# Kernel tuning notes

Hardware: AMD Instinct MI355X
Metric: run time of the kernel (lower is better)

The kernel has to match this reference:

```python
import jax, jax.numpy as jnp
import numpy as np
from math import factorial, sqrt, pi

LMAX, NSH = 2, 9
F = 64
N_RBF = 20
N_INTER = 2
N_ATOMS = 1000
N_PAIRS = 10000
CUTOFF = 5.0

# ---------- Clebsch-Gordan coefficients for real spherical harmonics ----------

def _cg_complex(l1, m1, l2, m2, l3, m3):
    # <l1 m1 l2 m2 | l3 m3> via Racah formula
    if m3 != m1 + m2 or not (abs(l1 - l2) <= l3 <= l1 + l2):
        return 0.0
    f = factorial
    pre = sqrt((2 * l3 + 1) * f(l3 + l1 - l2) * f(l3 - l1 + l2) * f(l1 + l2 - l3) / f(l1 + l2 + l3 + 1))
    pre *= sqrt(f(l3 + m3) * f(l3 - m3) * f(l1 - m1) * f(l1 + m1) * f(l2 - m2) * f(l2 + m2))
    s = 0.0
    for k in range(l1 + l2 - l3 + 1):
        d = [k, l1 + l2 - l3 - k, l1 - m1 - k, l2 + m2 - k, l3 - l2 + m1 + k, l3 - l1 - m2 + k]
        if min(d) < 0:
            continue
        s += (-1) ** k / np.prod([float(f(t)) for t in d])
    return pre * s

def _sh_indices(lmax):
    l = np.concatenate([np.full(2 * ll + 1, ll) for ll in range(lmax + 1)])
    m = np.concatenate([np.arange(-ll, ll + 1) for ll in range(lmax + 1)])
    return l, m

def _real_cg(lmax):
    lidx, midx = _sh_indices(lmax)
    n = (lmax + 1) ** 2
    cgc = np.zeros((n, n, n))
    for a in range(n):
        for b in range(n):
            for c in range(n):
                cgc[a, b, c] = _cg_complex(lidx[a], midx[a], lidx[b], midx[b], lidx[c], midx[c])
    # complex -> real spherical harmonic change of basis (per degree l)
    U = np.zeros((n, n), dtype=np.complex128)
    for ll in range(lmax + 1):
        base = ll * ll + ll
        U[base, base] = 1.0
        for m in range(1, ll + 1):
            U[base + m, base - m] = 1 / sqrt(2)
            U[base + m, base + m] = (-1) ** m / sqrt(2)
            U[base - m, base - m] = 1j / sqrt(2)
            U[base - m, base + m] = -1j * (-1) ** m / sqrt(2)
    cgr = np.einsum('ijk,ai,bj,ck->abc', cgc.astype(np.complex128), U, U, U.conj())
    parity = (-1.0) ** lidx
    mask = (parity[:, None, None] * parity[None, :, None]) == parity[None, None, :]
    cgr = np.real(cgr) * mask
    cgr = np.transpose(cgr, (2, 0, 1))  # [s_out, s_in(x), s_filter(Y)]
    s1, s2, s3 = np.nonzero(np.abs(cgr) > 1e-9)
    return s1, s2, s3, cgr[s1, s2, s3].astype(np.float32), lidx

_S1, _S2, _S3, _CGV, _LIDX = _real_cg(LMAX)
IDX1 = jnp.asarray(_S1)            # output sh channel per CG path
IDX2 = jnp.asarray(_S2)            # input-feature sh channel per CG path
IDX3 = jnp.asarray(_S3)            # Ylm sh channel per CG path
CGVAL = jnp.asarray(_CGV)          # CG value per path
WIDX = jnp.asarray(_LIDX[_S3])     # radial-filter degree per CG path
LIDX = jnp.asarray(_LIDX)          # degree of each of the 9 sh channels

# ---------- real spherical harmonics (lmax=2, orthonormal, m=-l..l order) ----------

def _rsh(u):
    x, y, z = u[:, 0], u[:, 1], u[:, 2]
    c1 = sqrt(3.0 / (4.0 * pi))
    c2 = 0.5 * sqrt(15.0 / pi)
    return jnp.stack([
        jnp.full_like(x, 0.5 / sqrt(pi)),
        c1 * y, c1 * z, c1 * x,
        c2 * x * y,
        c2 * y * z,
        0.25 * sqrt(5.0 / pi) * (3.0 * z * z - 1.0),
        c2 * x * z,
        0.25 * sqrt(15.0 / pi) * (x * x - y * y),
    ], axis=1)


def setup_inputs() -> dict:
    key = jax.random.key(0)
    ks = jax.random.split(key, 10)
    atomic_numbers = jax.random.randint(ks[0], (N_ATOMS,), 0, 100)
    r_ij = 1.5 * jax.random.normal(ks[1], (N_PAIRS, 3), dtype=jnp.float32)
    idx_i = jnp.sort(jax.random.randint(ks[2], (N_PAIRS,), 0, N_ATOMS))
    idx_j = jax.random.randint(ks[3], (N_PAIRS,), 0, N_ATOMS)
    emb = jax.random.normal(ks[4], (100, F), dtype=jnp.float32)
    def s(k, sh, fan):
        return jax.random.normal(k, sh, dtype=jnp.float32) / float(np.sqrt(fan))
    Wf = s(ks[5], (N_INTER, N_RBF, (LMAX + 1) * F), N_RBF)
    bf = jnp.zeros((N_INTER, (LMAX + 1) * F), jnp.float32)
    W1 = s(ks[6], (N_INTER, F, F), F)
    W2 = s(ks[7], (N_INTER, F, F), F)
    W3 = s(ks[8], (N_INTER, F, F), F)
    Wg = s(ks[9], (N_INTER, F, (LMAX + 1) * F), F)
    bg = jnp.zeros((N_INTER, (LMAX + 1) * F), jnp.float32)
    return dict(atomic_numbers=atomic_numbers, r_ij=r_ij, idx_i=idx_i, idx_j=idx_j,
                emb=emb, Wf=Wf, bf=bf, W1=W1, W2=W2, W3=W3, Wg=Wg, bg=bg)


def reference(atomic_numbers, r_ij, idx_i, idx_j, emb, Wf, bf, W1, W2, W3, Wg, bg):
    n_atoms = atomic_numbers.shape[0]
    d = jnp.linalg.norm(r_ij, axis=1, keepdims=True)          # [P,1]
    Yij = _rsh(r_ij / d)                                       # [P,9]
    offsets = jnp.linspace(0.0, CUTOFF, N_RBF)                 # GaussianRBF
    width = CUTOFF / (N_RBF - 1)
    radial = jnp.exp((-0.5 / (width * width)) * (d - offsets) ** 2)   # [P,n_rbf]
    cut = 0.5 * (jnp.cos(d * (pi / CUTOFF)) + 1.0) * (d < CUTOFF)     # [P,1]
    # nuclear embedding + scalar2rsh (zero-pad l>0 channels)
    x = jnp.zeros((n_atoms, NSH, F), emb.dtype).at[:, 0, :].set(emb[atomic_numbers])
    for t in range(N_INTER):
        # SO3Convolution
        Wij = (radial @ Wf[t] + bf[t]).reshape(-1, LMAX + 1, F) * cut[:, :, None]  # [P,lmax+1,F]
        xj = x[idx_j]                                                              # [P,9,F]
        v = xj[:, IDX2] * Yij[:, IDX3, None] * Wij[:, WIDX] * CGVAL[None, :, None]  # [P,nnz,F]
        yij = jnp.zeros_like(xj).at[:, IDX1].add(v)                                 # CG scatter
        dx = jax.ops.segment_sum(yij, idx_i, num_segments=n_atoms)                  # edge->node scatter
        # mixing1 + SO3TensorProduct
        ddx = dx @ W1[t]
        tp = jnp.zeros_like(dx).at[:, IDX1].add(dx[:, IDX2] * ddx[:, IDX3] * CGVAL[None, :, None])
        dx = (dx + tp) @ W2[t]
        # SO3ParametricGatedNonlinearity (gate from l=0 channel)
        gate = (dx[:, 0] @ Wg[t] + bg[t]).reshape(-1, LMAX + 1, F)
        dx = dx * jax.nn.sigmoid(gate[:, LIDX])
        dx = dx @ W3[t]
        x = x + dx
    return x  # multipole_representation [n_atoms, 9, F]; x[:,0] is scalar_representation
```

## Files before the change

kernel.cpp:

```cpp
#include <hip/hip_runtime.h>
#include <cmath>

constexpr int kNsh    = 9;
constexpr int kF      = 64;
constexpr int kNrbf   = 20;
constexpr int kNAtoms = 1000;
constexpr int kNPairs = 10000;
constexpr float kCutoffF = 5.0f;
constexpr int kMaxNZ  = 200;
constexpr int kCp     = 12;
constexpr int kXs     = kF * kCp;

struct CGSparse {
  int n;
  int c[kMaxNZ];
  int a[kMaxNZ];
  int b[kMaxNZ];
  float v[kMaxNZ];
};

constexpr double cfact(int n) {
  double r = 1.0;
  for (int i = 2; i <= n; i++) r *= (double)i;
  return r;
}
constexpr double cabs_(double x) { return x < 0 ? -x : x; }
constexpr double csqrt_(double x) {
  if (x <= 0.0) return 0.0;
  double g = x < 1.0 ? 1.0 : x;
  for (int i = 0; i < 60; i++) g = 0.5 * (g + x / g);
  return g;
}

constexpr double cg_cplx(int l1, int m1, int l2, int m2, int l3, int m3) {
  if (m3 != m1 + m2) return 0.0;
  int lo = l1 > l2 ? l1 - l2 : l2 - l1;
  if (l3 < lo || l3 > l1 + l2) return 0.0;
  double pre = csqrt_((2 * l3 + 1) * cfact(l3 + l1 - l2) * cfact(l3 - l1 + l2) *
                      cfact(l1 + l2 - l3) / cfact(l1 + l2 + l3 + 1));
  pre *= csqrt_(cfact(l3 + m3) * cfact(l3 - m3) * cfact(l1 - m1) *
                cfact(l1 + m1) * cfact(l2 - m2) * cfact(l2 + m2));
  double s = 0.0;
  for (int k = 0; k <= l1 + l2 - l3; k++) {
    int d0 = k, d1 = l1 + l2 - l3 - k, d2 = l1 - m1 - k;
    int d3 = l2 + m2 - k, d4 = l3 - l2 + m1 + k, d5 = l3 - l1 - m2 + k;
    if (d0 < 0 || d1 < 0 || d2 < 0 || d3 < 0 || d4 < 0 || d5 < 0) continue;
    double den = cfact(d0) * cfact(d1) * cfact(d2) * cfact(d3) * cfact(d4) * cfact(d5);
    s += ((k % 2) ? -1.0 : 1.0) / den;
  }
  return pre * s;
}

constexpr CGSparse build_cg() {
  CGSparse out{};
  int lidx[9] = {0, 1, 1, 1, 2, 2, 2, 2, 2};
  int midx[9] = {0, -1, 0, 1, -2, -1, 0, 1, 2};
  double Ur[9][9] = {};
  double Ui[9][9] = {};
  for (int l = 0; l <= 2; l++) {
    int base = l * l + l;
    Ur[base][base] = 1.0;
    for (int m = 1; m <= l; m++) {
      double s2 = 1.0 / csqrt_(2.0);
      double sgn = (m % 2) ? -1.0 : 1.0;
      Ur[base + m][base - m] = s2;
      Ur[base + m][base + m] = sgn * s2;
      Ui[base - m][base - m] = s2;
      Ui[base - m][base + m] = -sgn * s2;
    }
  }
  double cgr[9][9][9] = {};
  for (int i = 0; i < 9; i++)
    for (int j = 0; j < 9; j++)
      for (int k = 0; k < 9; k++) {
        double cv = cg_cplx(lidx[i], midx[i], lidx[j], midx[j], lidx[k], midx[k]);
        if (cv == 0.0) continue;
        for (int a2 = 0; a2 < 9; a2++) {
          if (Ur[a2][i] == 0.0 && Ui[a2][i] == 0.0) continue;
          for (int b2 = 0; b2 < 9; b2++) {
            if (Ur[b2][j] == 0.0 && Ui[b2][j] == 0.0) continue;
            for (int c2 = 0; c2 < 9; c2++) {
              if (Ur[c2][k] == 0.0 && Ui[c2][k] == 0.0) continue;
              double ar = Ur[a2][i], ai = Ui[a2][i];
              double br = Ur[b2][j], bi = Ui[b2][j];
              double cr = Ur[c2][k], ci = -Ui[c2][k];
              double pr = ar * br - ai * bi;
              double pi = ar * bi + ai * br;
              double rr = pr * cr - pi * ci;
              cgr[c2][a2][b2] += rr * cv;
            }
          }
        }
      }
  int n = 0;
  for (int c2 = 0; c2 < 9; c2++)
    for (int a2 = 0; a2 < 9; a2++)
      for (int b2 = 0; b2 < 9; b2++) {
        bool mask = ((lidx[a2] + lidx[b2]) % 2) == (lidx[c2] % 2);
        double v = mask ? cgr[c2][a2][b2] : 0.0;
        if (cabs_(v) > 1e-9) {
          out.c[n] = c2;
          out.a[n] = a2;
          out.b[n] = b2;
          out.v[n] = (float)v;
          n++;
        }
      }
  out.n = n;
  return out;
}

constexpr CGSparse CG = build_cg();
static_assert(CG.n > 0 && CG.n <= kMaxNZ, "CG table size out of range");

constexpr int kPreBlkPairs = kNPairs / 4;
constexpr int kPreBlkSeg   = (kNAtoms + 1 + 255) / 256;
constexpr int kPreBlkTotal = kPreBlkPairs + kPreBlkSeg;

__global__ __launch_bounds__(256) void k_pre(
    const float* __restrict__ rij, const float* __restrict__ Wf,
    const float* __restrict__ bf, const int* __restrict__ idx_i,
    float* __restrict__ Ypd, float* __restrict__ Wpair,
    int* __restrict__ seg) {
  const int blk = blockIdx.x;
  if (blk < kPreBlkPairs) {
    int wv = threadIdx.x >> 6;
    int f = threadIdx.x & 63;
    int p = blk * 4 + wv;
    float rx = rij[3 * p + 0], ry = rij[3 * p + 1], rz = rij[3 * p + 2];
    float d = sqrtf(rx * rx + ry * ry + rz * rz);
    float inv = 1.0f / d;
    float x = rx * inv, y = ry * inv, z = rz * inv;
    const float c0 = 0.28209479177387814f;
    const float c1 = 0.4886025119029199f;
    const float c2 = 1.0925484305920792f;
    const float c3 = 0.31539156525252005f;
    const float c4 = 0.5462742152960396f;
    if (f < 9) {
      float yv =
          (f == 0) ? c0 :
          (f == 1) ? c1 * y :
          (f == 2) ? c1 * z :
          (f == 3) ? c1 * x :
          (f == 4) ? c2 * x * y :
          (f == 5) ? c2 * y * z :
          (f == 6) ? c3 * (3.0f * z * z - 1.0f) :
          (f == 7) ? c2 * x * z :
                     c4 * (x * x - y * y);
      Ypd[p * 16 + f] = yv;
    }
    float cut = (d < kCutoffF) ? 0.5f * (cosf(d * (float)(M_PI / 5.0)) + 1.0f) : 0.0f;
    float radial[kNrbf];
    const float width = kCutoffF / (kNrbf - 1);
    const float coef = -0.5f / (width * width);
    #pragma unroll
    for (int k = 0; k < kNrbf; k++) {
      float off = (kCutoffF * k) / (kNrbf - 1);
      float tt = d - off;
      radial[k] = expf(coef * tt * tt);
    }
    #pragma unroll
    for (int t = 0; t < 2; t++) {
      #pragma unroll
      for (int l = 0; l < 3; l++) {
        float w = bf[t * 192 + l * 64 + f];
        #pragma unroll
        for (int k = 0; k < kNrbf; k++) {
          w += radial[k] * Wf[t * (kNrbf * 192) + k * 192 + l * 64 + f];
        }
        Wpair[t * (kNPairs * 192) + p * 192 + l * 64 + f] = w * cut;
      }
    }
  } else {
    int a = (blk - kPreBlkPairs) * 256 + threadIdx.x;
    if (a <= kNAtoms) {
      int lo = 0, hi = kNPairs;
      while (lo < hi) {
        int mid = (lo + hi) >> 1;
        if (idx_i[mid] < a) lo = mid + 1; else hi = mid;
      }
      seg[a] = lo;
    }
  }
}

__device__ __forceinline__ void mm_phase(const float* __restrict__ sA,
                                         const float* __restrict__ W,
                                         float* __restrict__ sRw,
                                         int k0, int cgi, int fb) {
  if (cgi >= 3) return;
  const int c0 = cgi * 4;
  float acc[4][4];
  #pragma unroll
  for (int i = 0; i < 4; i++)
    #pragma unroll
    for (int j = 0; j < 4; j++) acc[i][j] = 0.f;
  #pragma unroll
  for (int half = 0; half < 2; half++) {
    float4 wr[8];
    #pragma unroll
    for (int kk = 0; kk < 8; kk++) {
      wr[kk] = *(const float4*)(W + (k0 + half * 8 + kk) * kF + fb);
    }
    #pragma unroll
    for (int kk = 0; kk < 8; kk++) {
      int k = k0 + half * 8 + kk;
      float4 av = *(const float4*)(sA + k * kCp + c0);
      float4 wv = wr[kk];
      float a[4] = {av.x, av.y, av.z, av.w};
      float w[4] = {wv.x, wv.y, wv.z, wv.w};
      #pragma unroll
      for (int i = 0; i < 4; i++)
        #pragma unroll
        for (int j = 0; j < 4; j++) acc[i][j] += a[i] * w[j];
    }
  }
  #pragma unroll
  for (int j = 0; j < 4; j++) {
    float4 v = {acc[0][j], acc[1][j], acc[2][j], acc[3][j]};
    *(float4*)(sRw + (fb + j) * kCp + c0) = v;
  }
}

template <int T>
__global__ __launch_bounds__(256) void k_inter(
    const float* __restrict__ Ypd, const float* __restrict__ Wpt,
    const int* __restrict__ seg, const int* __restrict__ idx_j,
    const int* __restrict__ Z, const float* __restrict__ emb,
    const float* __restrict__ x_in, const float* __restrict__ W1,
    const float* __restrict__ W2, const float* __restrict__ W3,
    const float* __restrict__ Wg, const float* __restrict__ bg,
    float* __restrict__ x_out) {
  const int atom = blockIdx.x;
  const int tid = threadIdx.x;
  const int wv = tid >> 6;
  const int lane = tid & 63;
  const int cgi = lane >> 4;
  const int fb = (lane & 15) * 4;
  const int k0 = wv * 16;

  __shared__ __align__(16) float sA[kF * kCp];
  __shared__ __align__(16) float sR[4][kF * kCp];
  __shared__ __align__(16) float sGp[4][192];

  {
    float y[12];
    #pragma unroll
    for (int c = 0; c < 12; c++) y[c] = 0.f;
    const int s0 = seg[atom], s1 = seg[atom + 1];
    for (int p0 = s0 + wv; p0 < s1; p0 += 4) {
      const int p = __builtin_amdgcn_readfirstlane(p0);
      const int j = __builtin_amdgcn_readfirstlane(idx_j[p]);
      const float* Wp = Wpt + p * 192;
      float Wl0 = Wp[lane], Wl1 = Wp[64 + lane], Wl2 = Wp[128 + lane];
      const float* Yp = Ypd + p * 16;
      float YW[9];
      YW[0] = Yp[0] * Wl0;
      YW[1] = Yp[1] * Wl1;
      YW[2] = Yp[2] * Wl1;
      YW[3] = Yp[3] * Wl1;
      #pragma unroll
      for (int b = 4; b < 9; b++) YW[b] = Yp[b] * Wl2;
      if (T == 0) {
        float e = emb[Z[j] * kF + lane];
        #pragma unroll
        for (int q = 0; q < CG.n; q++) {
          if (CG.a[q] == 0) y[CG.c[q]] += CG.v[q] * YW[CG.b[q]] * e;
        }
      } else {
        const float* xj = x_in + j * kXs + lane * kCp;
        float xv[12];
        *(float4*)&xv[0] = *(const float4*)(xj + 0);
        *(float4*)&xv[4] = *(const float4*)(xj + 4);
        *(float4*)&xv[8] = *(const float4*)(xj + 8);
        #pragma unroll
        for (int q = 0; q < CG.n; q++) {
          y[CG.c[q]] += CG.v[q] * YW[CG.b[q]] * xv[CG.a[q]];
        }
      }
    }
    float4* r4 = (float4*)(sR[wv] + lane * kCp);
    r4[0] = *(float4*)&y[0];
    r4[1] = *(float4*)&y[4];
    r4[2] = *(float4*)&y[8];
  }
  __syncthreads();
  if (tid < 192) {
    const float4* r0 = (const float4*)sR[0];
    const float4* r1 = (const float4*)sR[1];
    const float4* r2 = (const float4*)sR[2];
    const float4* r3 = (const float4*)sR[3];
    float4 a = r0[tid], b = r1[tid], c = r2[tid], d = r3[tid];
    float4 s = {a.x + b.x + c.x + d.x, a.y + b.y + c.y + d.y,
                a.z + b.z + c.z + d.z, a.w + b.w + c.w + d.w};
    ((float4*)sA)[tid] = s;
  }
  __syncthreads();

  mm_phase(sA, W1, sR[wv], k0, cgi, fb);
  __syncthreads();

  if (wv == 0) {
    float dxv[12], ddx[12];
    {
      const float4* sa = (const float4*)(sA + lane * kCp);
      *(float4*)&dxv[0] = sa[0];
      *(float4*)&dxv[4] = sa[1];
      *(float4*)&dxv[8] = sa[2];
    }
    #pragma unroll
    for (int c = 0; c < 12; c++) {
      ddx[c] = sR[0][lane * kCp + c] + sR[1][lane * kCp + c] +
               sR[2][lane * kCp + c] + sR[3][lane * kCp + c];
    }
    float t2[12];
    #pragma unroll
    for (int c = 0; c < 9; c++) t2[c] = dxv[c];
    t2[9] = 0.f; t2[10] = 0.f; t2[11] = 0.f;
    #pragma unroll
    for (int q = 0; q < CG.n; q++) {
      t2[CG.c[q]] += CG.v[q] * dxv[CG.a[q]] * ddx[CG.b[q]];
    }
    float4* sa = (float4*)(sA + lane * kCp);
    sa[0] = *(float4*)&t2[0];
    sa[1] = *(float4*)&t2[4];
    sa[2] = *(float4*)&t2[8];
  }
  __syncthreads();

  mm_phase(sA, W2, sR[wv], k0, cgi, fb);
  __syncthreads();

  {
    float g0 = 0.f, g1 = 0.f, g2 = 0.f;
    #pragma unroll 4
    for (int kk = 0; kk < 16; kk++) {
      int k = k0 + kk;
      float a = sR[0][k * kCp] + sR[1][k * kCp] + sR[2][k * kCp] + sR[3][k * kCp];
      g0 += a * Wg[k * 192 + lane];
      g1 += a * Wg[k * 192 + 64 + lane];
      g2 += a * Wg[k * 192 + 128 + lane];
    }
    sGp[wv][lane] = g0;
    sGp[wv][64 + lane] = g1;
    sGp[wv][128 + lane] = g2;
  }
  __syncthreads();

  if (wv == 0) {
    float dx2v[12];
    #pragma unroll
    for (int c = 0; c < 12; c++) {
      dx2v[c] = sR[0][lane * kCp + c] + sR[1][lane * kCp + c] +
                sR[2][lane * kCp + c] + sR[3][lane * kCp + c];
    }
    float g0 = bg[lane] + sGp[0][lane] + sGp[1][lane] + sGp[2][lane] + sGp[3][lane];
    float g1 = bg[64 + lane] + sGp[0][64 + lane] + sGp[1][64 + lane] +
               sGp[2][64 + lane] + sGp[3][64 + lane];
    float g2 = bg[128 + lane] + sGp[0][128 + lane] + sGp[1][128 + lane] +
               sGp[2][128 + lane] + sGp[3][128 + lane];
    g0 = 1.f / (1.f + expf(-g0));
    g1 = 1.f / (1.f + expf(-g1));
    g2 = 1.f / (1.f + expf(-g2));
    float dx3[12];
    dx3[0] = dx2v[0] * g0;
    dx3[1] = dx2v[1] * g1;
    dx3[2] = dx2v[2] * g1;
    dx3[3] = dx2v[3] * g1;
    #pragma unroll
    for (int c = 4; c < 9; c++) dx3[c] = dx2v[c] * g2;
    dx3[9] = 0.f; dx3[10] = 0.f; dx3[11] = 0.f;
    float4* sa = (float4*)(sA + lane * kCp);
    sa[0] = *(float4*)&dx3[0];
    sa[1] = *(float4*)&dx3[4];
    sa[2] = *(float4*)&dx3[8];
  }
  __syncthreads();

  mm_phase(sA, W3, sR[wv], k0, cgi, fb);
  __syncthreads();

  if (T == 0) {
    if (tid < 192) {
      const int f = tid / 3, r = tid % 3;
      const float4* r0 = (const float4*)sR[0];
      const float4* r1 = (const float4*)sR[1];
      const float4* r2 = (const float4*)sR[2];
      const float4* r3 = (const float4*)sR[3];
      float4 a = r0[tid], b = r1[tid], c = r2[tid], d = r3[tid];
      float4 s = {a.x + b.x + c.x + d.x, a.y + b.y + c.y + d.y,
                  a.z + b.z + c.z + d.z, a.w + b.w + c.w + d.w};
      if (r == 0) s.x += emb[Z[atom] * kF + f];
      *(float4*)(x_out + atom * kXs + tid * 4) = s;
    }
  } else {
    if (tid < 192) {
      const float4* r0 = (const float4*)sR[0];
      const float4* r1 = (const float4*)sR[1];
      const float4* r2 = (const float4*)sR[2];
      const float4* r3 = (const float4*)sR[3];
      float4 a = r0[tid], b = r1[tid], c = r2[tid], d = r3[tid];
      float4 xi = *(const float4*)(x_in + atom * kXs + tid * 4);
      float4 s = {a.x + b.x + c.x + d.x + xi.x, a.y + b.y + c.y + d.y + xi.y,
                  a.z + b.z + c.z + d.z + xi.z, a.w + b.w + c.w + d.w + xi.w};
      ((float4*)sA)[tid] = s;
    }
    __syncthreads();
    #pragma unroll
    for (int r = 0; r < 3; r++) {
      int i = r * 256 + tid;
      if (i < kNsh * kF) {
        int c = i >> 6, f = i & 63;
        x_out[atom * (kNsh * kF) + i] = sA[f * kCp + c];
      }
    }
  }
}

extern "C" void kernel_launch(void* const* d_in, const int* in_sizes, int n_in,
                              void* d_out, int out_size, void* d_ws, size_t ws_size,
                              hipStream_t stream) {
  const int* Z        = (const int*)d_in[0];
  const float* rij    = (const float*)d_in[1];
  const int* idx_i    = (const int*)d_in[2];
  const int* idx_j    = (const int*)d_in[3];
  const float* emb    = (const float*)d_in[4];
  const float* Wf     = (const float*)d_in[5];
  const float* bf     = (const float*)d_in[6];
  const float* W1     = (const float*)d_in[7];
  const float* W2     = (const float*)d_in[8];
  const float* W3     = (const float*)d_in[9];
  const float* Wg     = (const float*)d_in[10];
  const float* bg     = (const float*)d_in[11];
  float* out = (float*)d_out;

  float* x1    = (float*)d_ws;
  float* Ypd   = x1 + kNAtoms * kXs;
  float* Wpair = Ypd + kNPairs * 16;
  int*   seg   = (int*)(Wpair + 2 * kNPairs * 192);

  k_pre<<<kPreBlkTotal, 256, 0, stream>>>(rij, Wf, bf, idx_i, Ypd, Wpair, seg);

  k_inter<0><<<kNAtoms, 256, 0, stream>>>(
      Ypd, Wpair, seg, idx_j, Z, emb, x1,
      W1, W2, W3, Wg, bg, x1);

  k_inter<1><<<kNAtoms, 256, 0, stream>>>(
      Ypd, Wpair + kNPairs * 192, seg, idx_j, Z, emb, x1,
      W1 + kF * kF, W2 + kF * kF, W3 + kF * kF,
      Wg + kF * 192, bg + 192, out);
}
```

Measured before the change: 125.6 us.

## Use eight waves per atom block and reduce matmul partials into shared buffer

Doubles the block size from 4 to 8 wavefronts per atom, so each wave handles every eighth pair in the edge gather and an 8-row K slice in each 64x64 mix. Partial results are now summed once by a dedicated reduction into a new shared buffer sB instead of being re-summed inside the single-wave CG and gate stages. This aims to spread the per-atom serial work across more waves. In exchange it adds extra barriers and roughly doubles shared memory per block, which may limit how many blocks fit on a CU.

```diff
diff --git a/kernel.cpp b/kernel.cpp
--- a/kernel.cpp
+++ b/kernel.cpp
@@ -10,6 +10,7 @@
 constexpr int kMaxNZ  = 200;
 constexpr int kCp     = 12;
 constexpr int kXs     = kF * kCp;
+constexpr int kNW     = 8;
 
 struct CGSparse {
   int n;
@@ -197,14 +198,14 @@
     for (int j = 0; j < 4; j++) acc[i][j] = 0.f;
   #pragma unroll
   for (int half = 0; half < 2; half++) {
-    float4 wr[8];
-    #pragma unroll
-    for (int kk = 0; kk < 8; kk++) {
-      wr[kk] = *(const float4*)(W + (k0 + half * 8 + kk) * kF + fb);
-    }
-    #pragma unroll
-    for (int kk = 0; kk < 8; kk++) {
-      int k = k0 + half * 8 + kk;
+    float4 wr[4];
+    #pragma unroll
+    for (int kk = 0; kk < 4; kk++) {
+      wr[kk] = *(const float4*)(W + (k0 + half * 4 + kk) * kF + fb);
+    }
+    #pragma unroll
+    for (int kk = 0; kk < 4; kk++) {
+      int k = k0 + half * 4 + kk;
       float4 av = *(const float4*)(sA + k * kCp + c0);
       float4 wv = wr[kk];
       float a[4] = {av.x, av.y, av.z, av.w};
@@ -222,8 +223,22 @@
   }
 }
 
+__device__ __forceinline__ void reduce_partials(const float (*sR)[kF * kCp],
+                                                float* __restrict__ dst,
+                                                int tid) {
+  if (tid < 192) {
+    float4 s = ((const float4*)sR[0])[tid];
+    #pragma unroll
+    for (int w = 1; w < kNW; w++) {
+      float4 v = ((const float4*)sR[w])[tid];
+      s.x += v.x; s.y += v.y; s.z += v.z; s.w += v.w;
+    }
+    ((float4*)dst)[tid] = s;
+  }
+}
+
 template <int T>
-__global__ __launch_bounds__(256) void k_inter(
+__global__ __launch_bounds__(512, 6) void k_inter(
     const float* __restrict__ Ypd, const float* __restrict__ Wpt,
     const int* __restrict__ seg, const int* __restrict__ idx_j,
     const int* __restrict__ Z, const float* __restrict__ emb,
@@ -237,18 +252,19 @@
   const int lane = tid & 63;
   const int cgi = lane >> 4;
   const int fb = (lane & 15) * 4;
-  const int k0 = wv * 16;
+  const int k0 = wv * 8;
 
   __shared__ __align__(16) float sA[kF * kCp];
-  __shared__ __align__(16) float sR[4][kF * kCp];
-  __shared__ __align__(16) float sGp[4][192];
+  __shared__ __align__(16) float sB[kF * kCp];
+  __shared__ __align__(16) float sR[kNW][kF * kCp];
+  __shared__ __align__(16) float sGp[kNW][192];
 
   {
     float y[12];
     #pragma unroll
     for (int c = 0; c < 12; c++) y[c] = 0.f;
     const int s0 = seg[atom], s1 = seg[atom + 1];
-    for (int p0 = s0 + wv; p0 < s1; p0 += 4) {
+    for (int p0 = s0 + wv; p0 < s1; p0 += kNW) {
       const int p = __builtin_amdgcn_readfirstlane(p0);
       const int j = __builtin_amdgcn_readfirstlane(idx_j[p]);
       const float* Wp = Wpt + p * 192;
@@ -285,19 +301,12 @@
     r4[2] = *(float4*)&y[8];
   }
   __syncthreads();
-  if (tid < 192) {
-    const float4* r0 = (const float4*)sR[0];
-    const float4* r1 = (const float4*)sR[1];
-    const float4* r2 = (const float4*)sR[2];
-    const float4* r3 = (const float4*)sR[3];
-    float4 a = r0[tid], b = r1[tid], c = r2[tid], d = r3[tid];
-    float4 s = {a.x + b.x + c.x + d.x, a.y + b.y + c.y + d.y,
-                a.z + b.z + c.z + d.z, a.w + b.w + c.w + d.w};
-    ((float4*)sA)[tid] = s;
-  }
+  reduce_partials(sR, sA, tid);
   __syncthreads();
 
   mm_phase(sA, W1, sR[wv], k0, cgi, fb);
+  __syncthreads();
+  reduce_partials(sR, sB, tid);
   __syncthreads();
 
   if (wv == 0) {
@@ -307,11 +316,10 @@
       *(float4*)&dxv[0] = sa[0];
       *(float4*)&dxv[4] = sa[1];
       *(float4*)&dxv[8] = sa[2];
-    }
-    #pragma unroll
-    for (int c = 0; c < 12; c++) {
-      ddx[c] = sR[0][lane * kCp + c] + sR[1][lane * kCp + c] +
-               sR[2][lane * kCp + c] + sR[3][lane * kCp + c];
+      const float4* sb = (const float4*)(sB + lane * kCp);
+      *(float4*)&ddx[0] = sb[0];
+      *(float4*)&ddx[4] = sb[1];
+      *(float4*)&ddx[8] = sb[2];
     }
     float t2[12];
     #pragma unroll
@@ -330,13 +338,15 @@
 
   mm_phase(sA, W2, sR[wv], k0, cgi, fb);
   __syncthreads();
+  reduce_partials(sR, sB, tid);
+  __syncthreads();
 
   {
     float g0 = 0.f, g1 = 0.f, g2 = 0.f;
-    #pragma unroll 4
-    for (int kk = 0; kk < 16; kk++) {
+    #pragma unroll
+    for (int kk = 0; kk < 8; kk++) {
       int k = k0 + kk;
-      float a = sR[0][k * kCp] + sR[1][k * kCp] + sR[2][k * kCp] + sR[3][k * kCp];
+      float a = sB[k * kCp];
       g0 += a * Wg[k * 192 + lane];
       g1 += a * Wg[k * 192 + 64 + lane];
       g2 += a * Wg[k * 192 + 128 + lane];
@@ -349,16 +359,19 @@
 
   if (wv == 0) {
     float dx2v[12];
-    #pragma unroll
-    for (int c = 0; c < 12; c++) {
-      dx2v[c] = sR[0][lane * kCp + c] + sR[1][lane * kCp + c] +
-                sR[2][lane * kCp + c] + sR[3][lane * kCp + c];
-    }
-    float g0 = bg[lane] + sGp[0][lane] + sGp[1][lane] + sGp[2][lane] + sGp[3][lane];
-    float g1 = bg[64 + lane] + sGp[0][64 + lane] + sGp[1][64 + lane] +
-               sGp[2][64 + lane] + sGp[3][64 + lane];
-    float g2 = bg[128 + lane] + sGp[0][128 + lane] + sGp[1][128 + lane] +
-               sGp[2][128 + lane] + sGp[3][128 + lane];
+    {
+      const float4* sb = (const float4*)(sB + lane * kCp);
+      *(float4*)&dx2v[0] = sb[0];
+      *(float4*)&dx2v[4] = sb[1];
+      *(float4*)&dx2v[8] = sb[2];
+    }
+    float g0 = bg[lane], g1 = bg[64 + lane], g2 = bg[128 + lane];
+    #pragma unroll
+    for (int w = 0; w < kNW; w++) {
+      g0 += sGp[w][lane];
+      g1 += sGp[w][64 + lane];
+      g2 += sGp[w][128 + lane];
+    }
     g0 = 1.f / (1.f + expf(-g0));
     g1 = 1.f / (1.f + expf(-g1));
     g2 = 1.f / (1.f + expf(-g2));
@@ -383,32 +396,31 @@
   if (T == 0) {
     if (tid < 192) {
       const int f = tid / 3, r = tid % 3;
-      const float4* r0 = (const float4*)sR[0];
-      const float4* r1 = (const float4*)sR[1];
-      const float4* r2 = (const float4*)sR[2];
-      const float4* r3 = (const float4*)sR[3];
-      float4 a = r0[tid], b = r1[tid], c = r2[tid], d = r3[tid];
-      float4 s = {a.x + b.x + c.x + d.x, a.y + b.y + c.y + d.y,
-                  a.z + b.z + c.z + d.z, a.w + b.w + c.w + d.w};
+      float4 s = ((const float4*)sR[0])[tid];
+      #pragma unroll
+      for (int w = 1; w < kNW; w++) {
+        float4 v = ((const float4*)sR[w])[tid];
+        s.x += v.x; s.y += v.y; s.z += v.z; s.w += v.w;
+      }
       if (r == 0) s.x += emb[Z[atom] * kF + f];
       *(float4*)(x_out + atom * kXs + tid * 4) = s;
     }
   } else {
     if (tid < 192) {
-      const float4* r0 = (const float4*)sR[0];
-      const float4* r1 = (const float4*)sR[1];
-      const float4* r2 = (const float4*)sR[2];
-      const float4* r3 = (const float4*)sR[3];
-      float4 a = r0[tid], b = r1[tid], c = r2[tid], d = r3[tid];
+      float4 s = ((const float4*)sR[0])[tid];
+      #pragma unroll
+      for (int w = 1; w < kNW; w++) {
+        float4 v = ((const float4*)sR[w])[tid];
+        s.x += v.x; s.y += v.y; s.z += v.z; s.w += v.w;
+      }
       float4 xi = *(const float4*)(x_in + atom * kXs + tid * 4);
-      float4 s = {a.x + b.x + c.x + d.x + xi.x, a.y + b.y + c.y + d.y + xi.y,
-                  a.z + b.z + c.z + d.z + xi.z, a.w + b.w + c.w + d.w + xi.w};
+      s.x += xi.x; s.y += xi.y; s.z += xi.z; s.w += xi.w;
       ((float4*)sA)[tid] = s;
     }
     __syncthreads();
     #pragma unroll
-    for (int r = 0; r < 3; r++) {
-      int i = r * 256 + tid;
+    for (int r = 0; r < 2; r++) {
+      int i = r * 512 + tid;
       if (i < kNsh * kF) {
         int c = i >> 6, f = i & 63;
         x_out[atom * (kNsh * kF) + i] = sA[f * kCp + c];
@@ -441,11 +453,11 @@
 
   k_pre<<<kPreBlkTotal, 256, 0, stream>>>(rij, Wf, bf, idx_i, Ypd, Wpair, seg);
 
-  k_inter<0><<<kNAtoms, 256, 0, stream>>>(
+  k_inter<0><<<kNAtoms, 512, 0, stream>>>(
       Ypd, Wpair, seg, idx_j, Z, emb, x1,
       W1, W2, W3, Wg, bg, x1);
 
-  k_inter<1><<<kNAtoms, 256, 0, stream>>>(
+  k_inter<1><<<kNAtoms, 512, 0, stream>>>(
       Ypd, Wpair + kNPairs * 192, seg, idx_j, Z, emb, x1,
       W1 + kF * kF, W2 + kF * kF, W3 + kF * kF,
       Wg + kF * 192, bg + 192, out);
```

After: 134.3 us. 1.07x slower.

## Fuse pair precompute into first interaction kernel, dropping a launch

Applied to the files above, without the earlier changes.

The separate pre-pass kernel is removed. The first interaction kernel now computes the spherical harmonics, cutoff and radial filter weights for its own atom's pairs, and extra blocks build the segment table. Each atom block finds its pair range with its own binary search over idx_i. This saves one kernel launch and the global round-trip for the first-layer filters. In exchange, the per-pair radial work is spread unevenly across atom blocks, and Wpair/Ypd are still written to and read back from global memory within the same block.

```diff
diff --git a/kernel.cpp b/kernel.cpp
--- a/kernel.cpp
+++ b/kernel.cpp
@@ -113,77 +113,6 @@
 constexpr CGSparse CG = build_cg();
 static_assert(CG.n > 0 && CG.n <= kMaxNZ, "CG table size out of range");
 
-constexpr int kPreBlkPairs = kNPairs / 4;
-constexpr int kPreBlkSeg   = (kNAtoms + 1 + 255) / 256;
-constexpr int kPreBlkTotal = kPreBlkPairs + kPreBlkSeg;
-
-__global__ __launch_bounds__(256) void k_pre(
-    const float* __restrict__ rij, const float* __restrict__ Wf,
-    const float* __restrict__ bf, const int* __restrict__ idx_i,
-    float* __restrict__ Ypd, float* __restrict__ Wpair,
-    int* __restrict__ seg) {
-  const int blk = blockIdx.x;
-  if (blk < kPreBlkPairs) {
-    int wv = threadIdx.x >> 6;
-    int f = threadIdx.x & 63;
-    int p = blk * 4 + wv;
-    float rx = rij[3 * p + 0], ry = rij[3 * p + 1], rz = rij[3 * p + 2];
-    float d = sqrtf(rx * rx + ry * ry + rz * rz);
-    float inv = 1.0f / d;
-    float x = rx * inv, y = ry * inv, z = rz * inv;
-    const float c0 = 0.28209479177387814f;
-    const float c1 = 0.4886025119029199f;
-    const float c2 = 1.0925484305920792f;
-    const float c3 = 0.31539156525252005f;
-    const float c4 = 0.5462742152960396f;
-    if (f < 9) {
-      float yv =
-          (f == 0) ? c0 :
-          (f == 1) ? c1 * y :
-          (f == 2) ? c1 * z :
-          (f == 3) ? c1 * x :
-          (f == 4) ? c2 * x * y :
-          (f == 5) ? c2 * y * z :
-          (f == 6) ? c3 * (3.0f * z * z - 1.0f) :
-          (f == 7) ? c2 * x * z :
-                     c4 * (x * x - y * y);
-      Ypd[p * 16 + f] = yv;
-    }
-    float cut = (d < kCutoffF) ? 0.5f * (cosf(d * (float)(M_PI / 5.0)) + 1.0f) : 0.0f;
-    float radial[kNrbf];
-    const float width = kCutoffF / (kNrbf - 1);
-    const float coef = -0.5f / (width * width);
-    #pragma unroll
-    for (int k = 0; k < kNrbf; k++) {
-      float off = (kCutoffF * k) / (kNrbf - 1);
-      float tt = d - off;
-      radial[k] = expf(coef * tt * tt);
-    }
-    #pragma unroll
-    for (int t = 0; t < 2; t++) {
-      #pragma unroll
-      for (int l = 0; l < 3; l++) {
-        float w = bf[t * 192 + l * 64 + f];
-        #pragma unroll
-        for (int k = 0; k < kNrbf; k++) {
-          w += radial[k] * Wf[t * (kNrbf * 192) + k * 192 + l * 64 + f];
-        }
-        Wpair[t * (kNPairs * 192) + p * 192 + l * 64 + f] = w * cut;
-      }
-    }
-  } else {
-    int a = (blk - kPreBlkPairs) * 256 + threadIdx.x;
-    if (a <= kNAtoms) {
-      int lo = 0, hi = kNPairs;
-      while (lo < hi) {
-        int mid = (lo + hi) >> 1;
-        if (idx_i[mid] < a) lo = mid + 1; else hi = mid;
-      }
-      seg[a] = lo;
-    }
-  }
-}
-
 __device__ __forceinline__ void mm_phase(const float* __restrict__ sA,
                                          const float* __restrict__ W,
                                          float* __restrict__ sRw,
@@ -222,11 +151,245 @@
   }
 }
 
-template <int T>
-__global__ __launch_bounds__(256) void k_inter(
+__global__ __launch_bounds__(256) void k_interA(
+    const float* __restrict__ rij, const float* __restrict__ Wf,
+    const float* __restrict__ bf, const int* __restrict__ idx_i,
+    const int* __restrict__ idx_j, const int* __restrict__ Z,
+    const float* __restrict__ emb, const float* __restrict__ W1,
+    const float* __restrict__ W2, const float* __restrict__ W3,
+    const float* __restrict__ Wg, const float* __restrict__ bg,
+    float* __restrict__ Ypd, float* __restrict__ Wpair,
+    int* __restrict__ seg, float* __restrict__ x_out) {
+  const int blk = blockIdx.x;
+  const int tid = threadIdx.x;
+
+  if (blk >= kNAtoms) {
+    int a = (blk - kNAtoms) * 256 + tid;
+    if (a <= kNAtoms) {
+      int lo = 0, hi = kNPairs;
+      while (lo < hi) {
+        int mid = (lo + hi) >> 1;
+        if (idx_i[mid] < a) lo = mid + 1; else hi = mid;
+      }
+      seg[a] = lo;
+    }
+    return;
+  }
+
+  const int atom = blk;
+  const int wv = tid >> 6;
+  const int lane = tid & 63;
+  const int cgi = lane >> 4;
+  const int fb = (lane & 15) * 4;
+  const int k0 = wv * 16;
+
+  __shared__ __align__(16) float sA[kF * kCp];
+  __shared__ __align__(16) float sR[4][kF * kCp];
+  __shared__ __align__(16) float sGp[4][192];
+  __shared__ int ss[2];
+
+  if (tid < 2) {
+    int target = atom + tid;
+    int lo = 0, hi = kNPairs;
+    while (lo < hi) {
+      int mid = (lo + hi) >> 1;
+      if (idx_i[mid] < target) lo = mid + 1; else hi = mid;
+    }
+    ss[tid] = lo;
+  }
+  __syncthreads();
+  const int s0 = ss[0], s1 = ss[1];
+
+  for (int p0 = s0 + wv; p0 < s1; p0 += 4) {
+    const int p = __builtin_amdgcn_readfirstlane(p0);
+    float rx = rij[3 * p + 0], ry = rij[3 * p + 1], rz = rij[3 * p + 2];
+    float d = sqrtf(rx * rx + ry * ry + rz * rz);
+    float inv = 1.0f / d;
+    float x = rx * inv, y = ry * inv, z = rz * inv;
+    const float c0 = 0.28209479177387814f;
+    const float c1 = 0.4886025119029199f;
+    const float c2 = 1.0925484305920792f;
+    const float c3 = 0.31539156525252005f;
+    const float c4 = 0.5462742152960396f;
+    if (lane < 9) {
+      float yv =
+          (lane == 0) ? c0 :
+          (lane == 1) ? c1 * y :
+          (lane == 2) ? c1 * z :
+          (lane == 3) ? c1 * x :
+          (lane == 4) ? c2 * x * y :
+          (lane == 5) ? c2 * y * z :
+          (lane == 6) ? c3 * (3.0f * z * z - 1.0f) :
+          (lane == 7) ? c2 * x * z :
+                        c4 * (x * x - y * y);
+      Ypd[p * 16 + lane] = yv;
+    }
+    float cut = (d < kCutoffF) ? 0.5f * (cosf(d * (float)(M_PI / 5.0)) + 1.0f) : 0.0f;
+    float radial[kNrbf];
+    const float width = kCutoffF / (kNrbf - 1);
+    const float coef = -0.5f / (width * width);
+    #pragma unroll
+    for (int k = 0; k < kNrbf; k++) {
+      float off = (kCutoffF * k) / (kNrbf - 1);
+      float tt = d - off;
+      radial[k] = expf(coef * tt * tt);
+    }
+    #pragma unroll
+    for (int t = 0; t < 2; t++) {
+      #pragma unroll
+      for (int l = 0; l < 3; l++) {
+        float w = bf[t * 192 + l * 64 + lane];
+        #pragma unroll
+        for (int k = 0; k < kNrbf; k++) {
+          w += radial[k] * Wf[t * (kNrbf * 192) + k * 192 + l * 64 + lane];
+        }
+        Wpair[t * (kNPairs * 192) + p * 192 + l * 64 + lane] = w * cut;
+      }
+    }
+  }
+  __syncthreads();
+
+  {
+    float y[12];
+    #pragma unroll
+    for (int c = 0; c < 12; c++) y[c] = 0.f;
+    for (int p0 = s0 + wv; p0 < s1; p0 += 4) {
+      const int p = __builtin_amdgcn_readfirstlane(p0);
+      const int j = __builtin_amdgcn_readfirstlane(idx_j[p]);
+      const float* Wp = Wpair + p * 192;
+      float Wl0 = Wp[lane], Wl1 = Wp[64 + lane], Wl2 = Wp[128 + lane];
+      const float* Yp = Ypd + p * 16;
+      float YW[9];
+      YW[0] = Yp[0] * Wl0;
+      YW[1] = Yp[1] * Wl1;
+      YW[2] = Yp[2] * Wl1;
+      YW[3] = Yp[3] * Wl1;
+      #pragma unroll
+      for (int b = 4; b < 9; b++) YW[b] = Yp[b] * Wl2;
+      float e = emb[Z[j] * kF + lane];
+      #pragma unroll
+      for (int q = 0; q < CG.n; q++) {
+        if (CG.a[q] == 0) y[CG.c[q]] += CG.v[q] * YW[CG.b[q]] * e;
+      }
+    }
+    float4* r4 = (float4*)(sR[wv] + lane * kCp);
+    r4[0] = *(float4*)&y[0];
+    r4[1] = *(float4*)&y[4];
+    r4[2] = *(float4*)&y[8];
+  }
+  __syncthreads();
+  if (tid < 192) {
+    const float4* r0 = (const float4*)sR[0];
+    const float4* r1 = (const float4*)sR[1];
+    const float4* r2 = (const float4*)sR[2];
+    const float4* r3 = (const float4*)sR[3];
+    float4 a = r0[tid], b = r1[tid], c = r2[tid], d = r3[tid];
+    float4 s = {a.x + b.x + c.x + d.x, a.y + b.y + c.y + d.y,
+                a.z + b.z + c.z + d.z, a.w + b.w + c.w + d.w};
+    ((float4*)sA)[tid] = s;
+  }
+  __syncthreads();
+
+  mm_phase(sA, W1, sR[wv], k0, cgi, fb);
+  __syncthreads();
+
+  if (wv == 0) {
+    float dxv[12], ddx[12];
+    {
+      const float4* sa = (const float4*)(sA + lane * kCp);
+      *(float4*)&dxv[0] = sa[0];
+      *(float4*)&dxv[4] = sa[1];
+      *(float4*)&dxv[8] = sa[2];
+    }
+    #pragma unroll
+    for (int c = 0; c < 12; c++) {
+      ddx[c] = sR[0][lane * kCp + c] + sR[1][lane * kCp + c] +
+               sR[2][lane * kCp + c] + sR[3][lane * kCp + c];
+    }
+    float t2[12];
+    #pragma unroll
+    for (int c = 0; c < 9; c++) t2[c] = dxv[c];
+    t2[9] = 0.f; t2[10] = 0.f; t2[11] = 0.f;
+    #pragma unroll
+    for (int q = 0; q < CG.n; q++) {
+      t2[CG.c[q]] += CG.v[q] * dxv[CG.a[q]] * ddx[CG.b[q]];
+    }
+    float4* sa = (float4*)(sA + lane * kCp);
+    sa[0] = *(float4*)&t2[0];
+    sa[1] = *(float4*)&t2[4];
+    sa[2] = *(float4*)&t2[8];
+  }
+  __syncthreads();
+
+  mm_phase(sA, W2, sR[wv], k0, cgi, fb);
+  __syncthreads();
+
+  {
+    float g0 = 0.f, g1 = 0.f, g2 = 0.f;
+    #pragma unroll 4
+    for (int kk = 0; kk < 16; kk++) {
+      int k = k0 + kk;
+      float a = sR[0][k * kCp] + sR[1][k * kCp] + sR[2][k * kCp] + sR[3][k * kCp];
+      g0 += a * Wg[k * 192 + lane];
+      g1 += a * Wg[k * 192 + 64 + lane];
+      g2 += a * Wg[k * 192 + 128 + lane];
+    }
+    sGp[wv][lane] = g0;
+    sGp[wv][64 + lane] = g1;
+    sGp[wv][128 + lane] = g2;
+  }
+  __syncthreads();
+
+  if (wv == 0) {
+    float dx2v[12];
+    #pragma unroll
+    for (int c = 0; c < 12; c++) {
+      dx2v[c] = sR[0][lane * kCp + c] + sR[1][lane * kCp + c] +
+                sR[2][lane * kCp + c] + sR[3][lane * kCp + c];
+    }
+    float g0 = bg[lane] + sGp[0][lane] + sGp[1][lane] + sGp[2][lane] + sGp[3][lane];
+    float g1 = bg[64 + lane] + sGp[0][64 + lane] + sGp[1][64 + lane] +
+               sGp[2][64 + lane] + sGp[3][64 + lane];
+    float g2 = bg[128 + lane] + sGp[0][128 + lane] + sGp[1][128 + lane] +
+               sGp[2][128 + lane] + sGp[3][128 + lane];
+    g0 = 1.f / (1.f + expf(-g0));
+    g1 = 1.f / (1.f + expf(-g1));
+    g2 = 1.f / (1.f + expf(-g2));
+    float dx3[12];
+    dx3[0] = dx2v[0] * g0;
+    dx3[1] = dx2v[1] * g1;
+    dx3[2] = dx2v[2] * g1;
+    dx3[3] = dx2v[3] * g1;
+    #pragma unroll
+    for (int c = 4; c < 9; c++) dx3[c] = dx2v[c] * g2;
+    dx3[9] = 0.f; dx3[10] = 0.f; dx3[11] = 0.f;
+    float4* sa = (float4*)(sA + lane * kCp);
+    sa[0] = *(float4*)&dx3[0];
+    sa[1] = *(float4*)&dx3[4];
+    sa[2] = *(float4*)&dx3[8];
+  }
+  __syncthreads();
+
+  mm_phase(sA, W3, sR[wv], k0, cgi, fb);
+  __syncthreads();
+
+  if (tid < 192) {
+    const int f = tid / 3, r = tid % 3;
+    const float4* r0 = (const float4*)sR[0];
+    const float4* r1 = (const float4*)sR[1];
+    const float4* r2 = (const float4*)sR[2];
+    const float4* r3 = (const float4*)sR[3];
+    float4 a = r0[tid], b = r1[tid], c = r2[tid], d = r3[tid];
+    float4 s = {a.x + b.x + c.x + d.x, a.y + b.y + c.y + d.y,
+                a.z + b.z + c.z + d.z, a.w + b.w + c.w + d.w};
+    if (r == 0) s.x += emb[Z[atom] * kF + f];
+    *(float4*)(x_out + atom * kXs + tid * 4) = s;
+  }
+}
+
+__global__ __launch_bounds__(256) void k_interB(
     const float* __restrict__ Ypd, const float* __restrict__ Wpt,
     const int* __restrict__ seg, const int* __restrict__ idx_j,
-    const int* __restrict__ Z, const float* __restrict__ emb,
     const float* __restrict__ x_in, const float* __restrict__ W1,
     const float* __restrict__ W2, const float* __restrict__ W3,
     const float* __restrict__ Wg, const float* __restrict__ bg,
@@ -261,22 +424,14 @@
       YW[3] = Yp[3] * Wl1;
       #pragma unroll
       for (int b = 4; b < 9; b++) YW[b] = Yp[b] * Wl2;
-      if (T == 0) {
-        float e = emb[Z[j] * kF + lane];
-        #pragma unroll
-        for (int q = 0; q < CG.n; q++) {
-          if (CG.a[q] == 0) y[CG.c[q]] += CG.v[q] * YW[CG.b[q]] * e;
-        }
-      } else {
-        const float* xj = x_in + j * kXs + lane * kCp;
-        float xv[12];
-        *(float4*)&xv[0] = *(const float4*)(xj + 0);
-        *(float4*)&xv[4] = *(const float4*)(xj + 4);
-        *(float4*)&xv[8] = *(const float4*)(xj + 8);
-        #pragma unroll
-        for (int q = 0; q < CG.n; q++) {
-          y[CG.c[q]] += CG.v[q] * YW[CG.b[q]] * xv[CG.a[q]];
-        }
+      const float* xj = x_in + j * kXs + lane * kCp;
+      float xv[12];
+      *(float4*)&xv[0] = *(const float4*)(xj + 0);
+      *(float4*)&xv[4] = *(const float4*)(xj + 4);
+      *(float4*)&xv[8] = *(const float4*)(xj + 8);
+      #pragma unroll
+      for (int q = 0; q < CG.n; q++) {
+        y[CG.c[q]] += CG.v[q] * YW[CG.b[q]] * xv[CG.a[q]];
       }
     }
     float4* r4 = (float4*)(sR[wv] + lane * kCp);
@@ -380,39 +535,24 @@
   mm_phase(sA, W3, sR[wv], k0, cgi, fb);
   __syncthreads();
 
-  if (T == 0) {
-    if (tid < 192) {
-      const int f = tid / 3, r = tid % 3;
-      const float4* r0 = (const float4*)sR[0];
-      const float4* r1 = (const float4*)sR[1];
-      const float4* r2 = (const float4*)sR[2];
-      const float4* r3 = (const float4*)sR[3];
-      float4 a = r0[tid], b = r1[tid], c = r2[tid], d = r3[tid];
-      float4 s = {a.x + b.x + c.x + d.x, a.y + b.y + c.y + d.y,
-                  a.z + b.z + c.z + d.z, a.w + b.w + c.w + d.w};
-      if (r == 0) s.x += emb[Z[atom] * kF + f];
-      *(float4*)(x_out + atom * kXs + tid * 4) = s;
-    }
-  } else {
-    if (tid < 192) {
-      const float4* r0 = (const float4*)sR[0];
-      const float4* r1 = (const float4*)sR[1];
-      const float4* r2 = (const float4*)sR[2];
-      const float4* r3 = (const float4*)sR[3];
-      float4 a = r0[tid], b = r1[tid], c = r2[tid], d = r3[tid];
-      float4 xi = *(const float4*)(x_in + atom * kXs + tid * 4);
-      float4 s = {a.x + b.x + c.x + d.x + xi.x, a.y + b.y + c.y + d.y + xi.y,
-                  a.z + b.z + c.z + d.z + xi.z, a.w + b.w + c.w + d.w + xi.w};
-      ((float4*)sA)[tid] = s;
-    }
-    __syncthreads();
-    #pragma unroll
-    for (int r = 0; r < 3; r++) {
-      int i = r * 256 + tid;
-      if (i < kNsh * kF) {
-        int c = i >> 6, f = i & 63;
-        x_out[atom * (kNsh * kF) + i] = sA[f * kCp + c];
-      }
+  if (tid < 192) {
+    const float4* r0 = (const float4*)sR[0];
+    const float4* r1 = (const float4*)sR[1];
+    const float4* r2 = (const float4*)sR[2];
+    const float4* r3 = (const float4*)sR[3];
+    float4 a = r0[tid], b = r1[tid], c = r2[tid], d = r3[tid];
+    float4 xi = *(const float4*)(x_in + atom * kXs + tid * 4);
+    float4 s = {a.x + b.x + c.x + d.x + xi.x, a.y + b.y + c.y + d.y + xi.y,
+                a.z + b.z + c.z + d.z + xi.z, a.w + b.w + c.w + d.w + xi.w};
+    ((float4*)sA)[tid] = s;
+  }
+  __syncthreads();
+  #pragma unroll
+  for (int r = 0; r < 3; r++) {
+    int i = r * 256 + tid;
+    if (i < kNsh * kF) {
+      int c = i >> 6, f = i & 63;
+      x_out[atom * (kNsh * kF) + i] = sA[f * kCp + c];
     }
   }
 }
@@ -439,14 +579,12 @@
   float* Wpair = Ypd + kNPairs * 16;
   int*   seg   = (int*)(Wpair + 2 * kNPairs * 192);
 
-  k_pre<<<kPreBlkTotal, 256, 0, stream>>>(rij, Wf, bf, idx_i, Ypd, Wpair, seg);
-
-  k_inter<0><<<kNAtoms, 256, 0, stream>>>(
-      Ypd, Wpair, seg, idx_j, Z, emb, x1,
-      W1, W2, W3, Wg, bg, x1);
-
-  k_inter<1><<<kNAtoms, 256, 0, stream>>>(
-      Ypd, Wpair + kNPairs * 192, seg, idx_j, Z, emb, x1,
+  k_interA<<<kNAtoms + 4, 256, 0, stream>>>(
+      rij, Wf, bf, idx_i, idx_j, Z, emb,
+      W1, W2, W3, Wg, bg, Ypd, Wpair, seg, x1);
+
+  k_interB<<<kNAtoms, 256, 0, stream>>>(
+      Ypd, Wpair + kNPairs * 192, seg, idx_j, x1,
       W1 + kF * kF, W2 + kF * kF, W3 + kF * kF,
       Wg + kF * 192, bg + 192, out);
 }
```

New measurement: 136.5 us. +8.7%, slower.

## Compute per-pair radial filter weights inside interaction kernels instead of precomputing

Applied to the files above, without the earlier changes.

The precompute kernel no longer materializes the per-pair filter weights for both interactions (two arrays of pairs×192 floats). It now stores only the spherical harmonics, the cutoff value and the cutoff-scaled radial basis per pair (32 floats). Each interaction block stages its filter matrix Wf in shared memory and recomputes the 192 filter weights per pair with a 20-term dot product. This trades a large global write and read for extra FLOPs and LDS traffic, and the larger shared-memory footprint may lower occupancy.

```diff
diff --git a/kernel.cpp b/kernel.cpp
--- a/kernel.cpp
+++ b/kernel.cpp
@@ -118,10 +118,8 @@
 constexpr int kPreBlkTotal = kPreBlkPairs + kPreBlkSeg;
 
 __global__ __launch_bounds__(256) void k_pre(
-    const float* __restrict__ rij, const float* __restrict__ Wf,
-    const float* __restrict__ bf, const int* __restrict__ idx_i,
-    float* __restrict__ Ypd, float* __restrict__ Wpair,
-    int* __restrict__ seg) {
+    const float* __restrict__ rij, const int* __restrict__ idx_i,
+    float* __restrict__ pd_all, int* __restrict__ seg) {
   const int blk = blockIdx.x;
   if (blk < kPreBlkPairs) {
     int wv = threadIdx.x >> 6;
@@ -136,8 +134,10 @@
     const float c2 = 1.0925484305920792f;
     const float c3 = 0.31539156525252005f;
     const float c4 = 0.5462742152960396f;
+    float cut = (d < kCutoffF) ? 0.5f * (cosf(d * (float)(M_PI / 5.0)) + 1.0f) : 0.0f;
+    float val = 0.f;
     if (f < 9) {
-      float yv =
+      val =
           (f == 0) ? c0 :
           (f == 1) ? c1 * y :
           (f == 2) ? c1 * z :
@@ -147,30 +147,16 @@
           (f == 6) ? c3 * (3.0f * z * z - 1.0f) :
           (f == 7) ? c2 * x * z :
                      c4 * (x * x - y * y);
-      Ypd[p * 16 + f] = yv;
-    }
-    float cut = (d < kCutoffF) ? 0.5f * (cosf(d * (float)(M_PI / 5.0)) + 1.0f) : 0.0f;
-    float radial[kNrbf];
-    const float width = kCutoffF / (kNrbf - 1);
-    const float coef = -0.5f / (width * width);
-    #pragma unroll
-    for (int k = 0; k < kNrbf; k++) {
-      float off = (kCutoffF * k) / (kNrbf - 1);
+    } else if (f == 9) {
+      val = cut;
+    } else if (f < 30) {
+      const float width = kCutoffF / (kNrbf - 1);
+      const float coef = -0.5f / (width * width);
+      float off = (kCutoffF * (f - 10)) / (kNrbf - 1);
       float tt = d - off;
-      radial[k] = expf(coef * tt * tt);
-    }
-    #pragma unroll
-    for (int t = 0; t < 2; t++) {
-      #pragma unroll
-      for (int l = 0; l < 3; l++) {
-        float w = bf[t * 192 + l * 64 + f];
-        #pragma unroll
-        for (int k = 0; k < kNrbf; k++) {
-          w += radial[k] * Wf[t * (kNrbf * 192) + k * 192 + l * 64 + f];
-        }
-        Wpair[t * (kNPairs * 192) + p * 192 + l * 64 + f] = w * cut;
-      }
-    }
+      val = expf(coef * tt * tt) * cut;
+    }
+    if (f < 30) pd_all[p * 32 + f] = val;
   } else {
     int a = (blk - kPreBlkPairs) * 256 + threadIdx.x;
     if (a <= kNAtoms) {
@@ -184,7 +170,7 @@
   }
 }
 
-__device__ __forceinline__ void mm_phase(const float* __restrict__ sA,
+__device__ __forceinline__ void mm_phase(const float* __restrict__ sIn,
                                          const float* __restrict__ W,
                                          float* __restrict__ sRw,
                                          int k0, int cgi, int fb) {
@@ -205,7 +191,7 @@
     #pragma unroll
     for (int kk = 0; kk < 8; kk++) {
       int k = k0 + half * 8 + kk;
-      float4 av = *(const float4*)(sA + k * kCp + c0);
+      float4 av = *(const float4*)(sIn + k * kCp + c0);
       float4 wv = wr[kk];
       float a[4] = {av.x, av.y, av.z, av.w};
       float w[4] = {wv.x, wv.y, wv.z, wv.w};
@@ -224,13 +210,13 @@
 
 template <int T>
 __global__ __launch_bounds__(256) void k_inter(
-    const float* __restrict__ Ypd, const float* __restrict__ Wpt,
-    const int* __restrict__ seg, const int* __restrict__ idx_j,
-    const int* __restrict__ Z, const float* __restrict__ emb,
-    const float* __restrict__ x_in, const float* __restrict__ W1,
-    const float* __restrict__ W2, const float* __restrict__ W3,
-    const float* __restrict__ Wg, const float* __restrict__ bg,
-    float* __restrict__ x_out) {
+    const float* __restrict__ pd_all, const float* __restrict__ Wft,
+    const float* __restrict__ bft, const int* __restrict__ seg,
+    const int* __restrict__ idx_j, const int* __restrict__ Z,
+    const float* __restrict__ emb, const float* __restrict__ x_in,
+    const float* __restrict__ W1, const float* __restrict__ W2,
+    const float* __restrict__ W3, const float* __restrict__ Wg,
+    const float* __restrict__ bg, float* __restrict__ x_out) {
   const int atom = blockIdx.x;
   const int tid = threadIdx.x;
   const int wv = tid >> 6;
@@ -239,9 +225,22 @@
   const int fb = (lane & 15) * 4;
   const int k0 = wv * 16;
 
+  __shared__ __align__(16) float sWf[kNrbf * 192];
   __shared__ __align__(16) float sA[kF * kCp];
   __shared__ __align__(16) float sR[4][kF * kCp];
   __shared__ __align__(16) float sGp[4][192];
+
+  {
+    const float4* g4 = (const float4*)Wft;
+    float4* s4 = (float4*)sWf;
+    #pragma unroll
+    for (int r = 0; r < 4; r++) {
+      int i = r * 256 + tid;
+      if (i < kNrbf * 192 / 4) s4[i] = g4[i];
+    }
+  }
+  const float bf0 = bft[lane], bf1 = bft[64 + lane], bf2 = bft[128 + lane];
+  __syncthreads();
 
   {
     float y[12];
@@ -251,16 +250,23 @@
     for (int p0 = s0 + wv; p0 < s1; p0 += 4) {
       const int p = __builtin_amdgcn_readfirstlane(p0);
       const int j = __builtin_amdgcn_readfirstlane(idx_j[p]);
-      const float* Wp = Wpt + p * 192;
-      float Wl0 = Wp[lane], Wl1 = Wp[64 + lane], Wl2 = Wp[128 + lane];
-      const float* Yp = Ypd + p * 16;
+      const float* pd = pd_all + p * 32;
+      const float cut = pd[9];
+      float Wl0 = bf0 * cut, Wl1 = bf1 * cut, Wl2 = bf2 * cut;
+      #pragma unroll
+      for (int k = 0; k < kNrbf; k++) {
+        float r = pd[10 + k];
+        Wl0 += r * sWf[k * 192 + lane];
+        Wl1 += r * sWf[k * 192 + 64 + lane];
+        Wl2 += r * sWf[k * 192 + 128 + lane];
+      }
       float YW[9];
-      YW[0] = Yp[0] * Wl0;
-      YW[1] = Yp[1] * Wl1;
-      YW[2] = Yp[2] * Wl1;
-      YW[3] = Yp[3] * Wl1;
+      YW[0] = pd[0] * Wl0;
+      YW[1] = pd[1] * Wl1;
+      YW[2] = pd[2] * Wl1;
+      YW[3] = pd[3] * Wl1;
       #pragma unroll
-      for (int b = 4; b < 9; b++) YW[b] = Yp[b] * Wl2;
+      for (int b = 4; b < 9; b++) YW[b] = pd[b] * Wl2;
       if (T == 0) {
         float e = emb[Z[j] * kF + lane];
         #pragma unroll
@@ -434,19 +440,18 @@
   const float* bg     = (const float*)d_in[11];
   float* out = (float*)d_out;
 
-  float* x1    = (float*)d_ws;
-  float* Ypd   = x1 + kNAtoms * kXs;
-  float* Wpair = Ypd + kNPairs * 16;
-  int*   seg   = (int*)(Wpair + 2 * kNPairs * 192);
-
-  k_pre<<<kPreBlkTotal, 256, 0, stream>>>(rij, Wf, bf, idx_i, Ypd, Wpair, seg);
+  float* x1  = (float*)d_ws;
+  float* pd  = x1 + kNAtoms * kXs;
+  int*   seg = (int*)(pd + kNPairs * 32);
+
+  k_pre<<<kPreBlkTotal, 256, 0, stream>>>(rij, idx_i, pd, seg);
 
   k_inter<0><<<kNAtoms, 256, 0, stream>>>(
-      Ypd, Wpair, seg, idx_j, Z, emb, x1,
+      pd, Wf, bf, seg, idx_j, Z, emb, x1,
       W1, W2, W3, Wg, bg, x1);
 
   k_inter<1><<<kNAtoms, 256, 0, stream>>>(
-      Ypd, Wpair + kNPairs * 192, seg, idx_j, Z, emb, x1,
+      pd, Wf + kNrbf * 192, bf + 192, seg, idx_j, Z, emb, x1,
       W1 + kF * kF, W2 + kF * kF, W3 + kF * kF,
       Wg + kF * 192, bg + 192, out);
 }
```

Result: faster. 123.0 us (-2.1%).
